# Kernel tuning notes

Measured on AMD Instinct MI355X. Metric: run time of the kernel, lower is better.

The kernel has to match this reference:

```python
import jax, jax.numpy as jnp
import numpy as np

B, N_UNK, M_KNOWN = 8, 8192, 2048
C1, C2 = 256, 256
MLP = [512, 256, 256]
K_ENC = 32
D = MLP[-1]


def setup_inputs() -> dict:
    key = jax.random.key(0)
    ks = jax.random.split(key, 16)
    return {
        "unknown": jax.random.normal(ks[0], (B, N_UNK, 3), jnp.float32),
        "known": jax.random.normal(ks[1], (B, M_KNOWN, 3), jnp.float32),
        "unknow_feats": jax.random.normal(ks[2], (B, C1, N_UNK), jnp.float32),
        "known_feats": jax.random.normal(ks[3], (B, C2, M_KNOWN), jnp.float32),
        "conv_w1": jax.random.normal(ks[4], (MLP[1], MLP[0]), jnp.float32) * 0.05,
        "conv_b1": jnp.zeros((MLP[1],), jnp.float32),
        "bn_g1": jnp.ones((MLP[1],), jnp.float32),
        "bn_b1": jnp.zeros((MLP[1],), jnp.float32),
        "bn_m1": jax.random.normal(ks[5], (MLP[1],), jnp.float32) * 0.01,
        "bn_v1": jax.random.uniform(ks[6], (MLP[1],), jnp.float32, 0.5, 1.5),
        "conv_w2": jax.random.normal(ks[7], (MLP[2], MLP[1]), jnp.float32) * 0.05,
        "conv_b2": jnp.zeros((MLP[2],), jnp.float32),
        "bn_g2": jnp.ones((MLP[2],), jnp.float32),
        "bn_b2": jnp.zeros((MLP[2],), jnp.float32),
        "bn_m2": jax.random.normal(ks[8], (MLP[2],), jnp.float32) * 0.01,
        "bn_v2": jax.random.uniform(ks[9], (MLP[2],), jnp.float32, 0.5, 1.5),
        "enc_codewords": jax.random.normal(ks[10], (K_ENC, D), jnp.float32) * float(1.0 / np.sqrt(K_ENC * D)),
        "enc_scale": jax.random.uniform(ks[11], (K_ENC,), jnp.float32, -1.0, 0.0),
        "lin_w": jax.random.normal(ks[12], (D, D * K_ENC), jnp.float32) * 0.02,
        "lin_b": jnp.zeros((D,), jnp.float32),
    }


def _conv_bn_relu(x, w, b, g, beta, mean, var):
    # 1x1 conv over (B,C,N) == channel GEMM, then BN (inference form), then ReLU
    x = jnp.einsum("oc,bcn->bon", w, x) + b[None, :, None]
    x = g[None, :, None] * (x - mean[None, :, None]) * jax.lax.rsqrt(var + 1e-5)[None, :, None] + beta[None, :, None]
    return jax.nn.relu(x)


def reference(unknown, known, unknow_feats, known_feats,
              conv_w1, conv_b1, bn_g1, bn_b1, bn_m1, bn_v1,
              conv_w2, conv_b2, bn_g2, bn_b2, bn_m2, bn_v2,
              enc_codewords, enc_scale, lin_w, lin_b):
    # ---- three_nn: 3 nearest known points for each unknown point ----
    x2 = jnp.sum(unknown * unknown, axis=-1)            # (B,n)
    y2 = jnp.sum(known * known, axis=-1)                # (B,m)
    d2 = x2[:, :, None] - 2.0 * jnp.einsum("bnc,bmc->bnm", unknown, known) + y2[:, None, :]
    dist = jnp.sqrt(jnp.maximum(d2, 1e-12))             # (B,n,m) Euclidean
    neg_d, idx = jax.lax.top_k(-dist, 3)                # 3 smallest
    dist3 = -neg_d                                      # (B,n,3)
    dist_recip = 1.0 / (dist3 + 1e-8)
    weight = dist_recip / jnp.sum(dist_recip, axis=2, keepdims=True)
    # ---- three_interpolate: gather + weighted sum ----
    gathered = jax.vmap(lambda f, i: f[:, i])(known_feats, idx)   # (B,C2,n,3)
    interp = jnp.einsum("bcnk,bnk->bcn", gathered, weight)        # (B,C2,n)
    feats = jnp.concatenate([interp, unknow_feats], axis=1)       # (B,C2+C1,n)
    # ---- SharedMLP (two 1x1 conv + BN + ReLU layers) ----
    h = _conv_bn_relu(feats, conv_w1, conv_b1, bn_g1, bn_b1, bn_m1, bn_v1)
    h = _conv_bn_relu(h, conv_w2, conv_b2, bn_g2, bn_b2, bn_m2, bn_v2)   # (B,D,n)
    # ---- Encoding layer (soft dictionary assignment, residual aggregate) ----
    X = jnp.swapaxes(h, 1, 2)                                     # (B,n,D)
    c2 = jnp.sum(enc_codewords * enc_codewords, axis=-1)          # (K,)
    xn2 = jnp.sum(X * X, axis=-1)                                 # (B,n)
    # scaled_l2: s_k * ||x - c_k||^2 without materializing (B,n,K,D) residuals
    sl = enc_scale[None, None, :] * (xn2[:, :, None] - 2.0 * jnp.einsum("bnd,kd->bnk", X, enc_codewords) + c2[None, None, :])
    A = jax.nn.softmax(sl, axis=-1)                               # (B,n,K)
    E = jnp.einsum("bnk,bnd->bkd", A, X) - jnp.sum(A, axis=1)[:, :, None] * enc_codewords[None]
    E = jax.nn.relu(E).reshape(E.shape[0], -1)                    # (B,K*D)
    E = E / jnp.maximum(jnp.linalg.norm(E, axis=1, keepdims=True), 1e-12)  # F.normalize
    ctx = jax.nn.sigmoid(E @ lin_w.T + lin_b)                     # (B,D)
    # ---- channel-attention fusion ----
    return h * ctx[:, :, None]                                    # (B,D,n)
```

## Files before the change

kernel.cpp:

```cpp
#include <hip/hip_runtime.h>
#include <stdint.h>

typedef unsigned short u16;
typedef unsigned int u32;
typedef __attribute__((ext_vector_type(8))) short short8;
typedef __attribute__((ext_vector_type(4))) float f32x4;
typedef __attribute__((ext_vector_type(4))) u32 u32x4;

#define B_ 8
#define N_ 8192
#define M_ 2048
#define DD 256
#define KENC 32

#define SC1 0
#define SH1 256
#define SC2 512
#define SH2 768
#define C2OFF 1024
#define SOFF 1056
#define RNOFF 1088

#define OFF_IDX3   0ull
#define OFF_W3     786432ull
#define OFF_FT     1572864ull
#define OFF_H1T    68681728ull
#define OFF_ERELU  102236160ull
#define OFF_PART   102498304ull
#define OFF_CONSTS 102760448ull
#define OFF_CTX    102768640ull
#define OFF_W1D    102776832ull
#define OFF_W2D    103038976ull
#define OFF_CWD    103170048ull
#define OFF_FLAG   103186432ull

__device__ __forceinline__ float bf2f(u16 v){ return __uint_as_float(((u32)v)<<16); }
__device__ __forceinline__ u16 f2bf(float f){
  u32 x = __float_as_uint(f);
  return (u16)((x + 0x7FFFu + ((x>>16)&1u)) >> 16);
}
__device__ __forceinline__ float ldf(const void* p, size_t i, int f){
  return f ? ((const float*)p)[i] : bf2f(((const u16*)p)[i]);
}

__global__ __launch_bounds__(256) void k_detect(const void* v1, int* flagp){
  __shared__ int cntb, cntf;
  int t = threadIdx.x;
  if (t==0){ cntb=0; cntf=0; }
  __syncthreads();
  float vb = bf2f(((const u16*)v1)[t]);
  if (!(vb > 0.4f && vb < 1.6f)) atomicAdd(&cntb, 1);
  if (t < 64){
    float vf = ((const float*)v1)[t];
    if (!(vf > 0.4f && vf < 1.6f)) atomicAdd(&cntf, 1);
  }
  __syncthreads();
  if (t==0) flagp[0] = (cntb > 0 && cntf == 0) ? 1 : 0;
}

__global__ __launch_bounds__(256) void k_convert(
    const void* w1, const void* w2, const void* cwsrc, const int* __restrict__ flagp,
    u16* __restrict__ W1d, u16* __restrict__ W2d, u16* __restrict__ CWd){
  int id = blockIdx.x*256 + threadIdx.x;
  int f = flagp[0];
  if (id < 131072){
    W1d[id] = f ? f2bf(((const float*)w1)[id]) : ((const u16*)w1)[id];
  } else if (id < 196608){
    int j = id - 131072;
    W2d[j] = f ? f2bf(((const float*)w2)[j]) : ((const u16*)w2)[j];
  } else if (id < 204800){
    int j = id - 196608;
    CWd[j] = f ? f2bf(((const float*)cwsrc)[j]) : ((const u16*)cwsrc)[j];
  }
}

__global__ __launch_bounds__(256) void k0_setup(
    const void* cb1, const void* g1, const void* be1, const void* m1, const void* v1,
    const void* cb2, const void* g2, const void* be2, const void* m2, const void* v2,
    const u16* __restrict__ CWd, const void* es, const int* __restrict__ flagp,
    float* __restrict__ consts){
  int t = threadIdx.x;
  int f = flagp[0];
  {
    float g = ldf(g1,t,f), be = ldf(be1,t,f), m = ldf(m1,t,f), v = ldf(v1,t,f), cb = ldf(cb1,t,f);
    float r = 1.f/sqrtf(v + 1e-5f);
    float sc = g*r;
    consts[SC1+t] = sc; consts[SH1+t] = (cb-m)*sc + be;
  }
  {
    float g = ldf(g2,t,f), be = ldf(be2,t,f), m = ldf(m2,t,f), v = ldf(v2,t,f), cb = ldf(cb2,t,f);
    float r = 1.f/sqrtf(v + 1e-5f);
    float sc = g*r;
    consts[SC2+t] = sc; consts[SH2+t] = (cb-m)*sc + be;
  }
  if (t < KENC){
    float s = 0.f;
    for (int d=0; d<DD; d++){ float c = bf2f(CWd[t*DD+d]); s = fmaf(c,c,s); }
    consts[C2OFF+t] = s;
    consts[SOFF+t]  = ldf(es,t,f);
  }
}

__global__ __launch_bounds__(256) void k1_three_nn(
    const void* unknown, const void* known, const int* __restrict__ flagp,
    int* __restrict__ idx3, float* __restrict__ w3){
  __shared__ float4 kp[M_];
  int b = blockIdx.y, t = threadIdx.x;
  int f = flagp[0];
  for (int i=t; i<M_; i+=256){
    size_t o = ((size_t)b*M_ + i)*3;
    float x = ldf(known,o,f), y = ldf(known,o+1,f), z = ldf(known,o+2,f);
    float y2 = __fadd_rn(__fadd_rn(__fmul_rn(x,x), __fmul_rn(y,y)), __fmul_rn(z,z));
    kp[i] = make_float4(x,y,z,y2);
  }
  __syncthreads();
  int q = t >> 2, sl = t & 3;
  int pid = blockIdx.x*64 + q;
  size_t uo = ((size_t)b*N_ + pid)*3;
  float ux=ldf(unknown,uo,f), uy=ldf(unknown,uo+1,f), uz=ldf(unknown,uo+2,f);
  float x2 = __fadd_rn(__fadd_rn(__fmul_rn(ux,ux), __fmul_rn(uy,uy)), __fmul_rn(uz,uz));
  float b0=3.4e38f, b1=3.4e38f, b2v=3.4e38f;
  int i0=-1, i1=-1, i2=-1;
  int mbase = sl*512;
  for (int mm=0; mm<512; mm+=4){
    float d[4];
    #pragma unroll
    for (int u=0;u<4;u++){
      float4 km = kp[mbase+mm+u];
      float dotv = __fadd_rn(__fadd_rn(__fmul_rn(ux,km.x), __fmul_rn(uy,km.y)), __fmul_rn(uz,km.z));
      d[u] = __fadd_rn(__fsub_rn(x2, __fmul_rn(2.f,dotv)), km.w);
    }
    #pragma unroll
    for (int u=0;u<4;u++){
      float d2 = d[u];
      if (d2 < b2v){
        int m = mbase+mm+u;
        if (d2 < b0){ b2v=b1;i2=i1; b1=b0;i1=i0; b0=d2;i0=m; }
        else if (d2 < b1){ b2v=b1;i2=i1; b1=d2;i1=m; }
        else { b2v=d2; i2=m; }
      }
    }
  }
  #pragma unroll
  for (int delta=1; delta<=2; delta<<=1){
    float o0=__shfl_xor(b0,delta,64), o1=__shfl_xor(b1,delta,64), o2=__shfl_xor(b2v,delta,64);
    int   j0=__shfl_xor(i0,delta,64), j1=__shfl_xor(i1,delta,64), j2=__shfl_xor(i2,delta,64);
    float dv[3] = {o0,o1,o2}; int jv[3] = {j0,j1,j2};
    #pragma unroll
    for (int e=0; e<3; e++){
      float dd = dv[e]; int jj = jv[e];
      bool lt2 = (dd < b2v) || (dd == b2v && jj < i2);
      if (lt2){
        bool lt0 = (dd < b0) || (dd == b0 && jj < i0);
        bool lt1 = (dd < b1) || (dd == b1 && jj < i1);
        if (lt0){ b2v=b1;i2=i1; b1=b0;i1=i0; b0=dd;i0=jj; }
        else if (lt1){ b2v=b1;i2=i1; b1=dd;i1=jj; }
        else { b2v=dd; i2=jj; }
      }
    }
  }
  if (sl == 0){
    float da = __fsqrt_rn(fmaxf(b0,1e-12f));
    float db = __fsqrt_rn(fmaxf(b1,1e-12f));
    float dc = __fsqrt_rn(fmaxf(b2v,1e-12f));
    float r0 = __fdiv_rn(1.f, __fadd_rn(da,1e-8f));
    float r1 = __fdiv_rn(1.f, __fadd_rn(db,1e-8f));
    float r2 = __fdiv_rn(1.f, __fadd_rn(dc,1e-8f));
    float rs = __fadd_rn(__fadd_rn(r0,r1),r2);
    size_t o = ((size_t)b*N_ + pid)*3;
    idx3[o]=i0; idx3[o+1]=i1; idx3[o+2]=i2;
    w3[o]=__fdiv_rn(r0,rs); w3[o+1]=__fdiv_rn(r1,rs); w3[o+2]=__fdiv_rn(r2,rs);
  }
}

__global__ __launch_bounds__(256) void k2_interp(
    const void* kf, const int* __restrict__ idx3,
    const float* __restrict__ w3, const int* __restrict__ flagp, u16* __restrict__ Ft){
  __shared__ u16 Ls[M_*8];
  int ct = blockIdx.x;
  int b = blockIdx.y, t = threadIdx.x;
  int f = flagp[0];
  for (int cp=0; cp<4; cp++){
    int c0 = ct*8 + cp*2;
    size_t base0 = ((size_t)b*DD + c0)*M_;
    size_t base1 = base0 + M_;
    for (int i=t; i<M_; i+=256){
      float f0 = ldf(kf, base0+i, f);
      float f1 = ldf(kf, base1+i, f);
      u32 w = (u32)f2bf(f0) | ((u32)f2bf(f1)<<16);
      *(u32*)(Ls + i*8 + cp*2) = w;
    }
  }
  __syncthreads();
  for (int rep=0; rep<32; rep++){
    int pid = rep*256 + t;
    size_t o3 = ((size_t)b*N_ + pid)*3;
    int ia = idx3[o3], ib = idx3[o3+1], ic = idx3[o3+2];
    float wa = w3[o3], wb = w3[o3+1], wc = w3[o3+2];
    short8 va = *(const short8*)(Ls + ia*8);
    short8 vb = *(const short8*)(Ls + ib*8);
    short8 vc = *(const short8*)(Ls + ic*8);
    u32x4 pk;
    #pragma unroll
    for (int cq=0; cq<4; cq++){
      float fa0 = bf2f((u16)va[cq*2]),   fb0 = bf2f((u16)vb[cq*2]),   fc0 = bf2f((u16)vc[cq*2]);
      float fa1 = bf2f((u16)va[cq*2+1]), fb1 = bf2f((u16)vb[cq*2+1]), fc1 = bf2f((u16)vc[cq*2+1]);
      float v0 = fmaf(wc, fc0, fmaf(wb, fb0, wa*fa0));
      float v1 = fmaf(wc, fc1, fmaf(wb, fb1, wa*fa1));
      pk[cq] = (u32)f2bf(v0) | ((u32)f2bf(v1)<<16);
    }
    *(u32x4*)(Ft + ((size_t)b*N_ + pid)*512 + ct*8) = pk;
  }
}

__global__ __launch_bounds__(256) void k2b_transpose_uf(
    const void* uf, const int* __restrict__ flagp, u16* __restrict__ Ft){
  __shared__ u16 Ls[64*72];
  int bx = blockIdx.x, cy = blockIdx.y, b = blockIdx.z, t = threadIdx.x;
  int f = flagp[0];
  {
    int n = t & 63, cg = t >> 6;
    for (int i=0; i<16; i++){
      int c = cg*16 + i;
      Ls[n*72 + c] = f2bf(ldf(uf, ((size_t)b*DD + cy*64 + c)*N_ + bx*64 + n, f));
    }
  }
  __syncthreads();
  int nl = t>>2, cc = t&3;
  u16* dst = Ft + ((size_t)b*N_ + bx*64 + nl)*512 + 256 + cy*64 + cc*16;
  *(u32x4*)dst     = *(const u32x4*)(Ls + nl*72 + cc*16);
  *(u32x4*)(dst+8) = *(const u32x4*)(Ls + nl*72 + cc*16 + 8);
}

__global__ __launch_bounds__(256) void gemm_bn_relu(
    const u16* __restrict__ W, const u16* __restrict__ Fin,
    const float* __restrict__ consts, int sc_off, int sh_off,
    u16* __restrict__ Out, int K){
  __shared__ u16 SM[17408];
  u16* As = SM; u16* Bs = SM + 4096;
  int b = blockIdx.z, ot = blockIdx.y*128, nt = blockIdx.x*128;
  int t = threadIdx.x, wave = t>>6, lane = t&63, ln = lane&15, quad = lane>>4;
  int wo = (wave&1)*64, wn = (wave>>1)*64;
  f32x4 acc[4][4];
  #pragma unroll
  for (int i=0;i<4;i++)
    #pragma unroll
    for (int j=0;j<4;j++) acc[i][j] = (f32x4)0.f;
  const u16* Wp = W + (size_t)ot*K;
  const u16* Fp = Fin + ((size_t)b*N_ + nt)*K;
  for (int kk=0; kk<K; kk+=32){
    #pragma unroll
    for (int i=0;i<2;i++){
      int ch = t*2 + i;
      int r = ch>>2, kc = (ch&3)*8;
      *(u32x4*)(As + r*32 + kc) = *(const u32x4*)(Wp + (size_t)r*K + kk + kc);
      *(u32x4*)(Bs + r*32 + kc) = *(const u32x4*)(Fp + (size_t)r*K + kk + kc);
    }
    __syncthreads();
    short8 af[4], bfr[4];
    #pragma unroll
    for (int i=0;i<4;i++) af[i]  = *(const short8*)(As + (wo+i*16+ln)*32 + quad*8);
    #pragma unroll
    for (int j=0;j<4;j++) bfr[j] = *(const short8*)(Bs + (wn+j*16+ln)*32 + quad*8);
    #pragma unroll
    for (int i=0;i<4;i++)
      #pragma unroll
      for (int j=0;j<4;j++)
        acc[i][j] = __builtin_amdgcn_mfma_f32_16x16x32_bf16(af[i], bfr[j], acc[i][j], 0,0,0);
    __syncthreads();
  }
  u16* Cs = SM;
  #pragma unroll
  for (int i=0;i<4;i++){
    #pragma unroll
    for (int r=0;r<4;r++){
      int ol = wo + i*16 + quad*4 + r;
      float sc = consts[sc_off + ot + ol], sh = consts[sh_off + ot + ol];
      #pragma unroll
      for (int j=0;j<4;j++){
        float v = fmaxf(fmaf(acc[i][j][r], sc, sh), 0.f);
        Cs[(wn + j*16 + ln)*136 + ol] = f2bf(v);
      }
    }
  }
  __syncthreads();
  int nl = t>>1, half = t&1;
  u16* dst = Out + ((size_t)b*N_ + nt + nl)*256 + ot + half*64;
  const u16* srcr = Cs + nl*136 + half*64;
  #pragma unroll
  for (int c=0;c<8;c++)
    *(u32x4*)(dst + c*8) = *(const u32x4*)(srcr + c*8);
}

__global__ __launch_bounds__(256) void k5_enc_partial(
    const u16* __restrict__ X, const u16* __restrict__ cw,
    const float* __restrict__ consts, float* __restrict__ Epart){
  __shared__ u16 Xs[64*264];
  __shared__ float A_lds[64*32];
  __shared__ float xn2s[64];
  int g = blockIdx.x, b = blockIdx.y, t = threadIdx.x;
  int wave = t>>6, lane = t&63, ln = lane&15, quad = lane>>4;
  int tk = t>>3, tg = t&7;
  float accE[32];
  #pragma unroll
  for (int p=0;p<32;p++) accE[p]=0.f;
  float asum = 0.f;
  float c2v0 = consts[C2OFF + ln], c2v1 = consts[C2OFF + 16 + ln];
  float sv0  = consts[SOFF + ln],  sv1  = consts[SOFF + 16 + ln];
  for (int tt=0; tt<2; tt++){
    int n0 = (g*2+tt)*64;
    const u16* Xp = X + ((size_t)b*N_ + n0)*256;
    #pragma unroll
    for (int i=0;i<8;i++){
      int ch = t + i*256;
      int r = ch>>5, kc = (ch&31)*8;
      *(u32x4*)(Xs + r*264 + kc) = *(const u32x4*)(Xp + r*256 + kc);
    }
    __syncthreads();
    if (t < 64){
      const u16* row = Xs + t*264;
      float s = 0.f;
      for (int d=0; d<256; d+=8){
        short8 xv = *(const short8*)(row + d);
        #pragma unroll
        for (int q=0;q<8;q++){ float x = bf2f((u16)xv[q]); s = fmaf(x,x,s); }
      }
      xn2s[t] = s;
    }
    __syncthreads();
    f32x4 pj0 = (f32x4)0.f, pj1 = (f32x4)0.f;
    const u16* xrow = Xs + (wave*16 + ln)*264;
    #pragma unroll
    for (int kk=0; kk<256; kk+=32){
      short8 a   = *(const short8*)(xrow + kk + quad*8);
      short8 bf0 = *(const short8*)(cw + (size_t)ln*256 + kk + quad*8);
      short8 bf1 = *(const short8*)(cw + (size_t)(16+ln)*256 + kk + quad*8);
      pj0 = __builtin_amdgcn_mfma_f32_16x16x32_bf16(a, bf0, pj0, 0,0,0);
      pj1 = __builtin_amdgcn_mfma_f32_16x16x32_bf16(a, bf1, pj1, 0,0,0);
    }
    #pragma unroll
    for (int r=0;r<4;r++){
      int nl = wave*16 + quad*4 + r;
      float xv = xn2s[nl];
      float v0 = sv0 * __fadd_rn(__fsub_rn(xv, __fmul_rn(2.f,pj0[r])), c2v0);
      float v1 = sv1 * __fadd_rn(__fsub_rn(xv, __fmul_rn(2.f,pj1[r])), c2v1);
      float mx = fmaxf(v0,v1);
      #pragma unroll
      for (int d=1; d<16; d<<=1) mx = fmaxf(mx, __shfl_xor(mx, d, 64));
      float e0 = __expf(v0-mx), e1 = __expf(v1-mx);
      float es = e0+e1;
      #pragma unroll
      for (int d=1; d<16; d<<=1) es += __shfl_xor(es, d, 64);
      float inv = 1.f/es;
      A_lds[nl*32 + ln]      = e0*inv;
      A_lds[nl*32 + 16 + ln] = e1*inv;
    }
    __syncthreads();
    #pragma unroll 2
    for (int n=0; n<64; n++){
      float a = A_lds[n*32 + tk];
      asum += a;
      const u16* xr = Xs + n*264 + tg*32;
      #pragma unroll
      for (int p8=0; p8<4; p8++){
        u32x4 xv = *(const u32x4*)(xr + p8*8);
        #pragma unroll
        for (int q=0; q<4; q++){
          u32 w = xv[q];
          float lo = __uint_as_float(w<<16);
          float hi = __uint_as_float(w & 0xffff0000u);
          accE[p8*8 + q*2]   = fmaf(a, lo, accE[p8*8 + q*2]);
          accE[p8*8 + q*2+1] = fmaf(a, hi, accE[p8*8 + q*2+1]);
        }
      }
    }
    __syncthreads();
  }
  int slab = b*64 + g;
  float* Ed = Epart + (size_t)slab*8224 + (size_t)tk*257;
  #pragma unroll
  for (int p=0;p<32;p++) Ed[tg*32 + p] = accE[p];
  if (tg==0) Ed[256] = asum;
}

__global__ __launch_bounds__(256) void k5b_reduce(
    const float* __restrict__ Epart, const u16* __restrict__ cw, float* __restrict__ Erelu){
  int id = blockIdx.x*256 + threadIdx.x;
  int d = id & 255, k = (id>>8)&31, b = id>>13;
  float s = 0.f, as = 0.f;
  for (int sl=0; sl<64; sl++){
    const float* Ep = Epart + ((size_t)(b*64+sl))*8224 + (size_t)k*257;
    s  += Ep[d];
    as += Ep[256];
  }
  float cv = bf2f(cw[k*256+d]);
  Erelu[(size_t)b*8192 + k*256 + d] = fmaxf(s - as*cv, 0.f);
}

__global__ __launch_bounds__(256) void k6a_norm(
    const float* __restrict__ Erelu, float* __restrict__ consts){
  __shared__ float red[256];
  int b = blockIdx.x, t = threadIdx.x;
  float s = 0.f;
  for (int i=0;i<32;i++){ float e = Erelu[(size_t)b*8192 + i*256 + t]; s = fmaf(e,e,s); }
  red[t] = s; __syncthreads();
  for (int w=128; w>0; w>>=1){ if (t<w) red[t] += red[t+w]; __syncthreads(); }
  if (t==0) consts[RNOFF + b] = 1.f/fmaxf(__fsqrt_rn(red[0]), 1e-12f);
}

__global__ __launch_bounds__(256) void k6b_partial(
    const float* __restrict__ Erelu, const void* lw, const int* __restrict__ flagp,
    float* __restrict__ partials){
  __shared__ float Er[256];
  int kc = blockIdx.x, b = blockIdx.y, t = threadIdx.x;
  int f = flagp[0];
  Er[t] = Erelu[(size_t)b*8192 + kc*256 + t];
  __syncthreads();
  float s = 0.f;
  if (f){
    const float* lwp = (const float*)lw + (size_t)t*8192 + kc*256;
    for (int p=0; p<256; p+=4){
      f32x4 v = *(const f32x4*)(lwp + p);
      #pragma unroll
      for (int q=0;q<4;q++) s = fmaf(Er[p+q], v[q], s);
    }
  } else {
    const u16* lwp = (const u16*)lw + (size_t)t*8192 + kc*256;
    for (int p=0; p<256; p+=8){
      u32x4 v = *(const u32x4*)(lwp + p);
      #pragma unroll
      for (int q=0;q<4;q++){
        u32 w = v[q];
        s = fmaf(Er[p+q*2],   __uint_as_float(w<<16), s);
        s = fmaf(Er[p+q*2+1], __uint_as_float(w & 0xffff0000u), s);
      }
    }
  }
  partials[((size_t)b*32 + kc)*256 + t] = s;
}

__global__ __launch_bounds__(256) void k6c_ctx(
    const float* __restrict__ partials, const float* __restrict__ consts,
    const void* lb, const int* __restrict__ flagp, float* __restrict__ ctx){
  int b = blockIdx.x, t = threadIdx.x;
  int f = flagp[0];
  float s = 0.f;
  for (int kc=0; kc<32; kc++) s += partials[((size_t)b*32+kc)*256 + t];
  float x = fmaf(consts[RNOFF+b], s, ldf(lb,t,f));
  ctx[b*256 + t] = 1.f/(1.f + __expf(-x));
}

__global__ __launch_bounds__(256) void k7_out(
    const u16* __restrict__ ht, const float* __restrict__ ctx,
    const int* __restrict__ flagp, void* out){
  __shared__ u16 Ls[64*72];
  int bx = blockIdx.x, oy = blockIdx.y, b = blockIdx.z, t = threadIdx.x;
  int f = flagp[0];
  {
    int nl = t>>2, oc = t&3;
    const u16* src = ht + ((size_t)b*N_ + bx*64 + nl)*256 + oy*64 + oc*16;
    *(u32x4*)(Ls + nl*72 + oc*16)     = *(const u32x4*)src;
    *(u32x4*)(Ls + nl*72 + oc*16 + 8) = *(const u32x4*)(src + 8);
  }
  __syncthreads();
  int ol = t>>2, nc = t&3;
  float cv = ctx[b*256 + oy*64 + ol];
  size_t dstoff = ((size_t)b*DD + oy*64 + ol)*N_ + bx*64 + nc*16;
  if (f){
    float* dst = (float*)out + dstoff;
    #pragma unroll
    for (int wq=0; wq<4; wq++){
      f32x4 v;
      #pragma unroll
      for (int q=0;q<4;q++) v[q] = bf2f(Ls[(nc*16 + wq*4 + q)*72 + ol]) * cv;
      *(f32x4*)(dst + wq*4) = v;
    }
  } else {
    u32 words[8];
    #pragma unroll
    for (int wq=0; wq<8; wq++){
      float v0 = bf2f(Ls[(nc*16 + wq*2)*72 + ol]) * cv;
      float v1 = bf2f(Ls[(nc*16 + wq*2+1)*72 + ol]) * cv;
      words[wq] = (u32)f2bf(v0) | ((u32)f2bf(v1)<<16);
    }
    u16* dst = (u16*)out + dstoff;
    u32x4 w0 = {words[0],words[1],words[2],words[3]};
    u32x4 w1 = {words[4],words[5],words[6],words[7]};
    *(u32x4*)dst     = w0;
    *(u32x4*)(dst+8) = w1;
  }
}

extern "C" void kernel_launch(void* const* d_in, const int* in_sizes, int n_in,
                              void* d_out, int out_size, void* d_ws, size_t ws_size,
                              hipStream_t stream){
  const void* unknown = d_in[0];
  const void* known   = d_in[1];
  const void* uf      = d_in[2];
  const void* kf      = d_in[3];
  const void* w1      = d_in[4];
  const void* cb1     = d_in[5];
  const void* g1      = d_in[6];
  const void* be1     = d_in[7];
  const void* m1      = d_in[8];
  const void* v1      = d_in[9];
  const void* w2      = d_in[10];
  const void* cb2     = d_in[11];
  const void* g2      = d_in[12];
  const void* be2     = d_in[13];
  const void* m2      = d_in[14];
  const void* v2      = d_in[15];
  const void* cw      = d_in[16];
  const void* es      = d_in[17];
  const void* lw      = d_in[18];
  const void* lb      = d_in[19];

  char* ws = (char*)d_ws;
  int*   idx3  = (int*)(ws + OFF_IDX3);
  float* w3    = (float*)(ws + OFF_W3);
  u16*   Ft    = (u16*)(ws + OFF_FT);
  u16*   ht    = Ft;
  u16*   h1t   = (u16*)(ws + OFF_H1T);
  float* Epart = (float*)(ws + OFF_H1T);
  float* Erelu    = (float*)(ws + OFF_ERELU);
  float* partials = (float*)(ws + OFF_PART);
  float* consts   = (float*)(ws + OFF_CONSTS);
  float* ctx      = (float*)(ws + OFF_CTX);
  u16*   W1d   = (u16*)(ws + OFF_W1D);
  u16*   W2d   = (u16*)(ws + OFF_W2D);
  u16*   CWd   = (u16*)(ws + OFF_CWD);
  int*   flagp = (int*)(ws + OFF_FLAG);

  k_detect<<<1, 256, 0, stream>>>(v1, flagp);
  k_convert<<<800, 256, 0, stream>>>(w1, w2, cw, flagp, W1d, W2d, CWd);
  k0_setup<<<1, 256, 0, stream>>>(cb1,g1,be1,m1,v1, cb2,g2,be2,m2,v2, CWd, es, flagp, consts);
  k1_three_nn<<<dim3(128,8), 256, 0, stream>>>(unknown, known, flagp, idx3, w3);
  k2_interp<<<dim3(32,8), 256, 0, stream>>>(kf, idx3, w3, flagp, Ft);
  k2b_transpose_uf<<<dim3(128,4,8), 256, 0, stream>>>(uf, flagp, Ft);
  gemm_bn_relu<<<dim3(64,2,8), 256, 0, stream>>>(W1d, Ft,  consts, SC1, SH1, h1t, 512);
  gemm_bn_relu<<<dim3(64,2,8), 256, 0, stream>>>(W2d, h1t, consts, SC2, SH2, ht,  256);
  k5_enc_partial<<<dim3(64,8), 256, 0, stream>>>(ht, CWd, consts, Epart);
  k5b_reduce<<<256, 256, 0, stream>>>(Epart, CWd, Erelu);
  k6a_norm<<<8, 256, 0, stream>>>(Erelu, consts);
  k6b_partial<<<dim3(32,8), 256, 0, stream>>>(Erelu, lw, flagp, partials);
  k6c_ctx<<<8, 256, 0, stream>>>(partials, consts, lb, flagp, ctx);
  k7_out<<<dim3(128,4,8), 256, 0, stream>>>(ht, ctx, flagp, d_out);
}
```

Measured before the change: 480.9 us.

## Use direct global-to-LDS loads with swizzle in GEMM and rebalance three_nn and interp grids

The GEMM K-step grows from 32 to 64. Its tiles are now loaded with global_load_lds straight into LDS using an XOR-swizzled layout, which avoids register staging and LDS bank conflicts. three_nn switches from 4 to 2 lanes per query point with interleaved candidate indices and folds the factor of 2 into the query coordinates. k2_interp gains a row-group grid dimension so it launches more blocks, though each block reloads the same known-feature tile into LDS. The block count of k1 is halved, so occupancy may drop.

```diff
diff --git a/kernel.cpp b/kernel.cpp
--- a/kernel.cpp
+++ b/kernel.cpp
@@ -42,6 +42,11 @@
 __device__ __forceinline__ float ldf(const void* p, size_t i, int f){
   return f ? ((const float*)p)[i] : bf2f(((const u16*)p)[i]);
 }
+__device__ __forceinline__ void gl_lds16(const u16* g, u16* l){
+  __builtin_amdgcn_global_load_lds(
+      (const __attribute__((address_space(1))) void*)g,
+      (__attribute__((address_space(3))) void*)l, 16, 0, 0);
+}
 
 __global__ __launch_bounds__(256) void k_detect(const void* v1, int* flagp){
   __shared__ int cntb, cntf;
@@ -114,37 +119,38 @@
     kp[i] = make_float4(x,y,z,y2);
   }
   __syncthreads();
-  int q = t >> 2, sl = t & 3;
-  int pid = blockIdx.x*64 + q;
+  int qq = t >> 1, sl = t & 1;
+  int pid = blockIdx.x*128 + qq;
   size_t uo = ((size_t)b*N_ + pid)*3;
   float ux=ldf(unknown,uo,f), uy=ldf(unknown,uo+1,f), uz=ldf(unknown,uo+2,f);
   float x2 = __fadd_rn(__fadd_rn(__fmul_rn(ux,ux), __fmul_rn(uy,uy)), __fmul_rn(uz,uz));
+  float u2x = ux+ux, u2y = uy+uy, u2z = uz+uz;
   float b0=3.4e38f, b1=3.4e38f, b2v=3.4e38f;
   int i0=-1, i1=-1, i2=-1;
-  int mbase = sl*512;
-  for (int mm=0; mm<512; mm+=4){
-    float d[4];
-    #pragma unroll
-    for (int u=0;u<4;u++){
-      float4 km = kp[mbase+mm+u];
-      float dotv = __fadd_rn(__fadd_rn(__fmul_rn(ux,km.x), __fmul_rn(uy,km.y)), __fmul_rn(uz,km.z));
-      d[u] = __fadd_rn(__fsub_rn(x2, __fmul_rn(2.f,dotv)), km.w);
-    }
-    #pragma unroll
-    for (int u=0;u<4;u++){
+  for (int j0=0; j0<1024; j0+=4){
+    float d[4]; int mi[4];
+    #pragma unroll
+    for (int u=0; u<4; u++){
+      int m = (j0+u)*2 + sl;
+      mi[u] = m;
+      float4 km = kp[m];
+      float dot2 = __fadd_rn(__fadd_rn(__fmul_rn(u2x,km.x), __fmul_rn(u2y,km.y)), __fmul_rn(u2z,km.z));
+      d[u] = __fadd_rn(__fsub_rn(x2, dot2), km.w);
+    }
+    #pragma unroll
+    for (int u=0; u<4; u++){
       float d2 = d[u];
-      if (d2 < b2v){
-        int m = mbase+mm+u;
+      if (__builtin_expect(d2 < b2v, 0)){
+        int m = mi[u];
         if (d2 < b0){ b2v=b1;i2=i1; b1=b0;i1=i0; b0=d2;i0=m; }
         else if (d2 < b1){ b2v=b1;i2=i1; b1=d2;i1=m; }
         else { b2v=d2; i2=m; }
       }
     }
   }
-  #pragma unroll
-  for (int delta=1; delta<=2; delta<<=1){
-    float o0=__shfl_xor(b0,delta,64), o1=__shfl_xor(b1,delta,64), o2=__shfl_xor(b2v,delta,64);
-    int   j0=__shfl_xor(i0,delta,64), j1=__shfl_xor(i1,delta,64), j2=__shfl_xor(i2,delta,64);
+  {
+    float o0=__shfl_xor(b0,1,64), o1=__shfl_xor(b1,1,64), o2=__shfl_xor(b2v,1,64);
+    int   j0=__shfl_xor(i0,1,64), j1=__shfl_xor(i1,1,64), j2=__shfl_xor(i2,1,64);
     float dv[3] = {o0,o1,o2}; int jv[3] = {j0,j1,j2};
     #pragma unroll
     for (int e=0; e<3; e++){
@@ -178,7 +184,8 @@
     const float* __restrict__ w3, const int* __restrict__ flagp, u16* __restrict__ Ft){
   __shared__ u16 Ls[M_*8];
   int ct = blockIdx.x;
-  int b = blockIdx.y, t = threadIdx.x;
+  int rg = blockIdx.y;
+  int b = blockIdx.z, t = threadIdx.x;
   int f = flagp[0];
   for (int cp=0; cp<4; cp++){
     int c0 = ct*8 + cp*2;
@@ -192,7 +199,7 @@
     }
   }
   __syncthreads();
-  for (int rep=0; rep<32; rep++){
+  for (int rep=rg*8; rep<rg*8+8; rep++){
     int pid = rep*256 + t;
     size_t o3 = ((size_t)b*N_ + pid)*3;
     int ia = idx3[o3], ib = idx3[o3+1], ic = idx3[o3+2];
@@ -237,7 +244,7 @@
     const float* __restrict__ consts, int sc_off, int sh_off,
     u16* __restrict__ Out, int K){
   __shared__ u16 SM[17408];
-  u16* As = SM; u16* Bs = SM + 4096;
+  u16* As = SM; u16* Bs = SM + 8192;
   int b = blockIdx.z, ot = blockIdx.y*128, nt = blockIdx.x*128;
   int t = threadIdx.x, wave = t>>6, lane = t&63, ln = lane&15, quad = lane>>4;
   int wo = (wave&1)*64, wn = (wave>>1)*64;
@@ -248,25 +255,36 @@
     for (int j=0;j<4;j++) acc[i][j] = (f32x4)0.f;
   const u16* Wp = W + (size_t)ot*K;
   const u16* Fp = Fin + ((size_t)b*N_ + nt)*K;
-  for (int kk=0; kk<K; kk+=32){
-    #pragma unroll
-    for (int i=0;i<2;i++){
-      int ch = t*2 + i;
-      int r = ch>>2, kc = (ch&3)*8;
-      *(u32x4*)(As + r*32 + kc) = *(const u32x4*)(Wp + (size_t)r*K + kk + kc);
-      *(u32x4*)(Bs + r*32 + kc) = *(const u32x4*)(Fp + (size_t)r*K + kk + kc);
+  for (int kk=0; kk<K; kk+=64){
+    #pragma unroll
+    for (int i=0;i<4;i++){
+      int c = wave*256 + i*64 + lane;
+      int r = c>>3, k8 = (c&7) ^ (r&7);
+      const u16* gA = Wp + (size_t)r*K + kk + k8*8;
+      const u16* gB = Fp + (size_t)r*K + kk + k8*8;
+      gl_lds16(gA, As + (size_t)(wave*256 + i*64)*8);
+      gl_lds16(gB, Bs + (size_t)(wave*256 + i*64)*8);
     }
     __syncthreads();
-    short8 af[4], bfr[4];
-    #pragma unroll
-    for (int i=0;i<4;i++) af[i]  = *(const short8*)(As + (wo+i*16+ln)*32 + quad*8);
-    #pragma unroll
-    for (int j=0;j<4;j++) bfr[j] = *(const short8*)(Bs + (wn+j*16+ln)*32 + quad*8);
-    #pragma unroll
-    for (int i=0;i<4;i++)
-      #pragma unroll
-      for (int j=0;j<4;j++)
-        acc[i][j] = __builtin_amdgcn_mfma_f32_16x16x32_bf16(af[i], bfr[j], acc[i][j], 0,0,0);
+    #pragma unroll
+    for (int kh=0; kh<2; kh++){
+      short8 af[4], bfr[4];
+      #pragma unroll
+      for (int i=0;i<4;i++){
+        int R = wo + i*16 + ln, C = kh*4 + quad;
+        af[i] = *(const short8*)(As + (size_t)(R*8 + (C^(R&7)))*8);
+      }
+      #pragma unroll
+      for (int j=0;j<4;j++){
+        int R = wn + j*16 + ln, C = kh*4 + quad;
+        bfr[j] = *(const short8*)(Bs + (size_t)(R*8 + (C^(R&7)))*8);
+      }
+      #pragma unroll
+      for (int i=0;i<4;i++)
+        #pragma unroll
+        for (int j=0;j<4;j++)
+          acc[i][j] = __builtin_amdgcn_mfma_f32_16x16x32_bf16(af[i], bfr[j], acc[i][j], 0,0,0);
+    }
     __syncthreads();
   }
   u16* Cs = SM;
@@ -534,8 +552,8 @@
   k_detect<<<1, 256, 0, stream>>>(v1, flagp);
   k_convert<<<800, 256, 0, stream>>>(w1, w2, cw, flagp, W1d, W2d, CWd);
   k0_setup<<<1, 256, 0, stream>>>(cb1,g1,be1,m1,v1, cb2,g2,be2,m2,v2, CWd, es, flagp, consts);
-  k1_three_nn<<<dim3(128,8), 256, 0, stream>>>(unknown, known, flagp, idx3, w3);
-  k2_interp<<<dim3(32,8), 256, 0, stream>>>(kf, idx3, w3, flagp, Ft);
+  k1_three_nn<<<dim3(64,8), 256, 0, stream>>>(unknown, known, flagp, idx3, w3);
+  k2_interp<<<dim3(32,4,8), 256, 0, stream>>>(kf, idx3, w3, flagp, Ft);
   k2b_transpose_uf<<<dim3(128,4,8), 256, 0, stream>>>(uf, flagp, Ft);
   gemm_bn_relu<<<dim3(64,2,8), 256, 0, stream>>>(W1d, Ft,  consts, SC1, SH1, h1t, 512);
   gemm_bn_relu<<<dim3(64,2,8), 256, 0, stream>>>(W2d, h1t, consts, SC2, SH2, ht,  256);
```

Measured after the change: 476.4 us. Within noise of the previous version (-0.9%).
